# Performance work log

Measured on AMD Instinct MI355X. Metric: run time of the kernel, lower is better.

The kernel has to match this reference:

```python
import jax, jax.numpy as jnp
import numpy as np

V, E, H, K = 100000, 256, 512, 7
T, B = 256, 128


def _lstm(Wih, Whh, bih, bhh, xs):
    # xs: [T, B, E] -> hs: [T, B, H]. PyTorch gate order: i, f, g, o.
    Bsz = xs.shape[1]
    Hd = Whh.shape[1]
    b = bih + bhh

    def step(carry, x):
        h, c = carry
        gates = x @ Wih.T + h @ Whh.T + b  # [B, 4H]
        i, f, g, o = jnp.split(gates, 4, axis=-1)
        c = jax.nn.sigmoid(f) * c + jax.nn.sigmoid(i) * jnp.tanh(g)
        h = jax.nn.sigmoid(o) * jnp.tanh(c)
        return (h, c), h

    init = (jnp.zeros((Bsz, Hd), xs.dtype), jnp.zeros((Bsz, Hd), xs.dtype))
    _, hs = jax.lax.scan(step, init, xs)
    return hs


def setup_inputs() -> dict:
    key = jax.random.key(0)
    ks = jax.random.split(key, 16)
    s = 0.02
    n = lambda k, shape: (jax.random.normal(k, shape, dtype=jnp.float32) * s)
    inp = {
        "inputData": jax.random.randint(ks[0], (T, B), 0, V),
        "labels": jax.random.randint(ks[1], (B, T), 0, K),
        "embed_table": jax.random.normal(ks[2], (V, E), dtype=jnp.float32),
        "Wih_f": n(ks[3], (4 * H, E)), "Whh_f": n(ks[4], (4 * H, H)),
        "bih_f": n(ks[5], (4 * H,)), "bhh_f": n(ks[6], (4 * H,)),
        "Wih_b": n(ks[7], (4 * H, E)), "Whh_b": n(ks[8], (4 * H, H)),
        "bih_b": n(ks[9], (4 * H,)), "bhh_b": n(ks[10], (4 * H,)),
        "lin_W": n(ks[11], (K, 2 * H)), "lin_b": n(ks[12], (K,)),
        "trans": n(ks[13], (K, K)),
        "start_trans": n(ks[14], (K,)),
        "end_trans": n(ks[15], (K,)),
    }
    return inp


def reference(inputData, labels, embed_table, Wih_f, Whh_f, bih_f, bhh_f,
              Wih_b, Whh_b, bih_b, bhh_b, lin_W, lin_b, trans, start_trans, end_trans):
    # Embedding + BiLSTM (seq-major, torch default batch_first=False)
    xs = embed_table[inputData]                        # [T, B, E]
    hs_f = _lstm(Wih_f, Whh_f, bih_f, bhh_f, xs)       # [T, B, H]
    hs_b = _lstm(Wih_b, Whh_b, bih_b, bhh_b, xs[::-1])[::-1]
    hs = jnp.concatenate([hs_f, hs_b], axis=-1)        # [T, B, 2H]
    emissions = hs @ lin_W.T + lin_b                   # [T, B, K]

    em = emissions.transpose(1, 0, 2)                  # [B, T, K] batch-first for CRF

    # --- CRF gold-path score (mask = all ones, include start/end transitions) ---
    emit_scores = jnp.take_along_axis(em, labels[..., None], axis=2)[..., 0]  # [B, T]
    score = (start_trans[labels[:, 0]]
             + emit_scores.sum(axis=1)
             + trans[labels[:, :-1], labels[:, 1:]].sum(axis=1)
             + end_trans[labels[:, -1]])               # [B]

    # --- CRF log-partition via forward algorithm (lax.scan over time) ---
    alpha0 = start_trans[None, :] + em[:, 0]           # [B, K]

    def fwd_step(alpha, e_t):  # e_t: [B, K]
        new = jax.nn.logsumexp(alpha[:, :, None] + trans[None, :, :] + e_t[:, None, :], axis=1)
        return new, None

    alphaT, _ = jax.lax.scan(fwd_step, alpha0, em[:, 1:].transpose(1, 0, 2))
    logZ = jax.nn.logsumexp(alphaT + end_trans[None, :], axis=1)  # [B]

    log_likelihood = (score - logZ).sum()
    return -log_likelihood
```

## Files before the change

### kernel.cpp

```cpp
#include <hip/hip_runtime.h>
#include <hip/hip_bf16.h>

#define TT 256
#define BB 128
#define EE 256
#define HH 512
#define KK 7
#define WLD 776

typedef short bf16x8 __attribute__((ext_vector_type(8)));
typedef float f32x4 __attribute__((ext_vector_type(4)));
typedef unsigned short u16x8 __attribute__((ext_vector_type(8)));

__device__ __forceinline__ unsigned short f2bf(float x) {
  unsigned u = __builtin_bit_cast(unsigned, x);
  u += 0x7FFFu + ((u >> 16) & 1u);
  return (unsigned short)(u >> 16);
}
__device__ __forceinline__ float bf2f(unsigned short b) {
  return __builtin_bit_cast(float, (unsigned)b << 16);
}

__device__ __forceinline__ bf16x8 gload_sc0(const unsigned short* p) {
  bf16x8 v;
  asm volatile("global_load_dwordx4 %0, %1, off sc0"
               : "=v"(v) : "v"(p) : "memory");
  return v;
}

__global__ __launch_bounds__(256) void embed_kernel(
    const int* __restrict__ ids, const float* __restrict__ emb,
    unsigned short* __restrict__ xsb) {
  const int t = blockIdx.x, tid = threadIdx.x;
  const int b = tid >> 1, half = tid & 1;
  const int id = ids[t * BB + b];
  const float4* src = (const float4*)(emb + (size_t)id * EE + half * 128);
  unsigned short* dst = xsb + ((size_t)t * BB + b) * EE + half * 128;
#pragma unroll
  for (int i = 0; i < 32; ++i) {
    const float4 v = src[i];
    ushort4 o;
    o.x = f2bf(v.x); o.y = f2bf(v.y); o.z = f2bf(v.z); o.w = f2bf(v.w);
    *(ushort4*)(dst + i * 4) = o;
  }
}

__global__ __launch_bounds__(128) void bilstm_kernel(
    const unsigned short* __restrict__ xsb,
    const float* __restrict__ Wih_f, const float* __restrict__ Whh_f,
    const float* __restrict__ bih_f, const float* __restrict__ bhh_f,
    const float* __restrict__ Wih_b, const float* __restrict__ Whh_b,
    const float* __restrict__ bih_b, const float* __restrict__ bhh_b,
    unsigned short* __restrict__ hbuf, unsigned short* __restrict__ hs,
    int* __restrict__ bar) {
  __shared__ unsigned short Wl[64][WLD];
  __shared__ float gt[2][2][4][64][4];
  __shared__ int sinfo[2];

  const int tid = threadIdx.x;
  if (tid == 0) {
    const unsigned xcd = __builtin_amdgcn_s_getreg(14356) & 7;
    sinfo[0] = (int)xcd;
    sinfo[1] = atomicAdd(&bar[256 + xcd * 32], 1);
  }
  __syncthreads();
  const int g = sinfo[0];
  const int slot = sinfo[1] & 31;
  const int dir = g >> 2;
  const int r0 = (g & 3) * 32;
  const int j0 = slot * 16;
  int* cnt = bar + g * 32;

  const float* Wih = dir ? Wih_b : Wih_f;
  const float* Whh = dir ? Whh_b : Whh_f;
  const float* bih = dir ? bih_b : bih_f;
  const float* bhh = dir ? bhh_b : bhh_f;

  for (int idx = tid; idx < 64 * 192; idx += 128) {
    const int r = idx / 192;
    const int k4 = (idx - r * 192) * 4;
    const int grow = (r >> 4) * HH + j0 + (r & 15);
    float4 v;
    if (k4 < EE) v = *(const float4*)(Wih + (size_t)grow * EE + k4);
    else v = *(const float4*)(Whh + (size_t)grow * HH + (k4 - EE));
    ushort4 o;
    o.x = f2bf(v.x); o.y = f2bf(v.y); o.z = f2bf(v.z); o.w = f2bf(v.w);
    *(ushort4*)&Wl[r][k4] = o;
  }
  const int lane = tid & 63, ln = lane & 15, kk = lane >> 4;
  const int kh = tid >> 6;

  const float bi_ = bih[0 * HH + j0 + ln] + bhh[0 * HH + j0 + ln];
  const float bf_ = bih[1 * HH + j0 + ln] + bhh[1 * HH + j0 + ln];
  const float bg_ = bih[2 * HH + j0 + ln] + bhh[2 * HH + j0 + ln];
  const float bo_ = bih[3 * HH + j0 + ln] + bhh[3 * HH + j0 + ln];

  const unsigned short* wlp0 = &Wl[0 * 16 + ln][kk * 8];
  const unsigned short* wlp1 = &Wl[1 * 16 + ln][kk * 8];
  const unsigned short* wlp2 = &Wl[2 * 16 + ln][kk * 8];
  const unsigned short* wlp3 = &Wl[3 * 16 + ln][kk * 8];

  float c[4] = {0.f, 0.f, 0.f, 0.f};
  __syncthreads();

  int target = 32;
  for (int s = 0; s < TT; ++s) {
    const int t = dir ? (TT - 1 - s) : s;
    const int p = s & 1;
    f32x4 a00 = {0,0,0,0}, a01 = a00, a02 = a00, a03 = a00;
    f32x4 a10 = a00, a11 = a00, a12 = a00, a13 = a00;

    bf16x8 hv0[12], hv1[12];
    const unsigned short* hbase =
        hbuf + ((size_t)(p * 8 + g) * 32) * HH + kk * 8;
    const unsigned short* hp0 = hbase + (size_t)ln * HH;
    const unsigned short* hp1 = hbase + (size_t)(16 + ln) * HH;
    if (s > 0) {
      if (kh == 0) {
#pragma unroll
        for (int i = 0; i < 4; ++i) {
          hv0[i] = gload_sc0(hp0 + i * 32);
          hv1[i] = gload_sc0(hp1 + i * 32);
        }
      } else {
#pragma unroll
        for (int i = 0; i < 12; ++i) {
          hv0[i] = gload_sc0(hp0 + (4 + i) * 32);
          hv1[i] = gload_sc0(hp1 + (4 + i) * 32);
        }
      }
    }
    if (kh == 0) {
      const unsigned short* xr0 = xsb + ((size_t)t * BB + r0 + ln) * EE + kk * 8;
      const unsigned short* xr1 = xr0 + 16 * EE;
#pragma unroll
      for (int kt = 0; kt < 8; ++kt) {
        const bf16x8 av0 = *(const bf16x8*)(xr0 + kt * 32);
        const bf16x8 av1 = *(const bf16x8*)(xr1 + kt * 32);
        const bf16x8 b0 = *(const bf16x8*)(wlp0 + kt * 32);
        const bf16x8 b1 = *(const bf16x8*)(wlp1 + kt * 32);
        const bf16x8 b2 = *(const bf16x8*)(wlp2 + kt * 32);
        const bf16x8 b3 = *(const bf16x8*)(wlp3 + kt * 32);
        a00 = __builtin_amdgcn_mfma_f32_16x16x32_bf16(av0, b0, a00, 0, 0, 0);
        a01 = __builtin_amdgcn_mfma_f32_16x16x32_bf16(av0, b1, a01, 0, 0, 0);
        a02 = __builtin_amdgcn_mfma_f32_16x16x32_bf16(av0, b2, a02, 0, 0, 0);
        a03 = __builtin_amdgcn_mfma_f32_16x16x32_bf16(av0, b3, a03, 0, 0, 0);
        a10 = __builtin_amdgcn_mfma_f32_16x16x32_bf16(av1, b0, a10, 0, 0, 0);
        a11 = __builtin_amdgcn_mfma_f32_16x16x32_bf16(av1, b1, a11, 0, 0, 0);
        a12 = __builtin_amdgcn_mfma_f32_16x16x32_bf16(av1, b2, a12, 0, 0, 0);
        a13 = __builtin_amdgcn_mfma_f32_16x16x32_bf16(av1, b3, a13, 0, 0, 0);
      }
    }
    if (s > 0) {
      asm volatile("s_waitcnt vmcnt(0)" ::: "memory");
      __builtin_amdgcn_sched_barrier(0);
      if (kh == 0) {
#pragma unroll
        for (int i = 0; i < 4; ++i) {
          const int kt = i;
          const bf16x8 b0 = *(const bf16x8*)(wlp0 + EE + kt * 32);
          const bf16x8 b1 = *(const bf16x8*)(wlp1 + EE + kt * 32);
          const bf16x8 b2 = *(const bf16x8*)(wlp2 + EE + kt * 32);
          const bf16x8 b3 = *(const bf16x8*)(wlp3 + EE + kt * 32);
          a00 = __builtin_amdgcn_mfma_f32_16x16x32_bf16(hv0[i], b0, a00, 0, 0, 0);
          a01 = __builtin_amdgcn_mfma_f32_16x16x32_bf16(hv0[i], b1, a01, 0, 0, 0);
          a02 = __builtin_amdgcn_mfma_f32_16x16x32_bf16(hv0[i], b2, a02, 0, 0, 0);
          a03 = __builtin_amdgcn_mfma_f32_16x16x32_bf16(hv0[i], b3, a03, 0, 0, 0);
          a10 = __builtin_amdgcn_mfma_f32_16x16x32_bf16(hv1[i], b0, a10, 0, 0, 0);
          a11 = __builtin_amdgcn_mfma_f32_16x16x32_bf16(hv1[i], b1, a11, 0, 0, 0);
          a12 = __builtin_amdgcn_mfma_f32_16x16x32_bf16(hv1[i], b2, a12, 0, 0, 0);
          a13 = __builtin_amdgcn_mfma_f32_16x16x32_bf16(hv1[i], b3, a13, 0, 0, 0);
        }
      } else {
#pragma unroll
        for (int i = 0; i < 12; ++i) {
          const int kt = 4 + i;
          const bf16x8 b0 = *(const bf16x8*)(wlp0 + EE + kt * 32);
          const bf16x8 b1 = *(const bf16x8*)(wlp1 + EE + kt * 32);
          const bf16x8 b2 = *(const bf16x8*)(wlp2 + EE + kt * 32);
          const bf16x8 b3 = *(const bf16x8*)(wlp3 + EE + kt * 32);
          a00 = __builtin_amdgcn_mfma_f32_16x16x32_bf16(hv0[i], b0, a00, 0, 0, 0);
          a01 = __builtin_amdgcn_mfma_f32_16x16x32_bf16(hv0[i], b1, a01, 0, 0, 0);
          a02 = __builtin_amdgcn_mfma_f32_16x16x32_bf16(hv0[i], b2, a02, 0, 0, 0);
          a03 = __builtin_amdgcn_mfma_f32_16x16x32_bf16(hv0[i], b3, a03, 0, 0, 0);
          a10 = __builtin_amdgcn_mfma_f32_16x16x32_bf16(hv1[i], b0, a10, 0, 0, 0);
          a11 = __builtin_amdgcn_mfma_f32_16x16x32_bf16(hv1[i], b1, a11, 0, 0, 0);
          a12 = __builtin_amdgcn_mfma_f32_16x16x32_bf16(hv1[i], b2, a12, 0, 0, 0);
          a13 = __builtin_amdgcn_mfma_f32_16x16x32_bf16(hv1[i], b3, a13, 0, 0, 0);
        }
      }
    }
    *(f32x4*)&gt[kh][0][0][lane][0] = a00;
    *(f32x4*)&gt[kh][0][1][lane][0] = a01;
    *(f32x4*)&gt[kh][0][2][lane][0] = a02;
    *(f32x4*)&gt[kh][0][3][lane][0] = a03;
    *(f32x4*)&gt[kh][1][0][lane][0] = a10;
    *(f32x4*)&gt[kh][1][1][lane][0] = a11;
    *(f32x4*)&gt[kh][1][2][lane][0] = a12;
    *(f32x4*)&gt[kh][1][3][lane][0] = a13;
    __syncthreads();
    {
      const int mu = kh;
      unsigned short* hw =
          hbuf + ((size_t)((p ^ 1) * 8 + g) * 32 + mu * 16 + kk * 4) * HH + j0 + ln;
      unsigned short* hsw =
          hs + ((size_t)t * BB + r0 + mu * 16 + kk * 4) * 1024 + dir * HH + j0 + ln;
#pragma unroll
      for (int r = 0; r < 4; ++r) {
        const float gi = gt[0][mu][0][lane][r] + gt[1][mu][0][lane][r] + bi_;
        const float gf = gt[0][mu][1][lane][r] + gt[1][mu][1][lane][r] + bf_;
        const float gg = gt[0][mu][2][lane][r] + gt[1][mu][2][lane][r] + bg_;
        const float go = gt[0][mu][3][lane][r] + gt[1][mu][3][lane][r] + bo_;
        const float si = 1.f / (1.f + __expf(-gi));
        const float sf = 1.f / (1.f + __expf(-gf));
        const float so = 1.f / (1.f + __expf(-go));
        const float gcl = fminf(fmaxf(gg, -30.f), 30.f);
        const float eg = __expf(-2.f * gcl);
        const float tg = (1.f - eg) / (1.f + eg);
        const float cn = fmaf(sf, c[r], si * tg);
        c[r] = cn;
        const float ccl = fminf(fmaxf(cn, -30.f), 30.f);
        const float ec = __expf(-2.f * ccl);
        const float tc = (1.f - ec) / (1.f + ec);
        const float hn = so * tc;
        const unsigned short hb = f2bf(hn);
        hw[(size_t)r * HH] = hb;
        hsw[(size_t)r * 1024] = hb;
      }
    }
    __syncthreads();
    if (tid == 0) {
      __hip_atomic_fetch_add(cnt, 1, __ATOMIC_RELAXED, __HIP_MEMORY_SCOPE_AGENT);
      while (__hip_atomic_load(cnt, __ATOMIC_RELAXED, __HIP_MEMORY_SCOPE_AGENT) <
             target) {
        __builtin_amdgcn_s_sleep(1);
      }
    }
    __syncthreads();
    target += 32;
  }
}

__global__ __launch_bounds__(256) void emissions_kernel(
    const unsigned short* __restrict__ hs, const float* __restrict__ linW,
    const float* __restrict__ linb, float* __restrict__ em) {
  const int t = blockIdx.x, tid = threadIdx.x;
  const int wv = tid >> 6, l = tid & 63;
  for (int b = wv; b < BB; b += 4) {
    const unsigned short* hr = hs + ((size_t)t * BB + b) * 1024 + l * 16;
    const u16x8 v0 = *(const u16x8*)(hr);
    const u16x8 v1 = *(const u16x8*)(hr + 8);
    float x[16];
#pragma unroll
    for (int j = 0; j < 8; ++j) {
      x[j] = bf2f(v0[j]);
      x[8 + j] = bf2f(v1[j]);
    }
    float acc[KK];
#pragma unroll
    for (int k = 0; k < KK; ++k) {
      const float* wr = linW + (size_t)k * 1024 + l * 16;
      float ssum = 0.f;
#pragma unroll
      for (int j = 0; j < 16; ++j) ssum = fmaf(x[j], wr[j], ssum);
      acc[k] = ssum;
    }
#pragma unroll
    for (int k = 0; k < KK; ++k) {
#pragma unroll
      for (int off = 32; off > 0; off >>= 1) acc[k] += __shfl_xor(acc[k], off);
    }
    if (l == 0) {
      float* o = em + ((size_t)b * TT + t) * KK;
#pragma unroll
      for (int k = 0; k < KK; ++k) o[k] = acc[k] + linb[k];
    }
  }
}

__global__ __launch_bounds__(64) void crf_kernel(
    const float* __restrict__ em, const int* __restrict__ lab,
    const float* __restrict__ trans, const float* __restrict__ st_,
    const float* __restrict__ en_, float* __restrict__ partial) {
  const int b = blockIdx.x;
  const int lane = threadIdx.x;
  __shared__ float tr[49], st[7], en[7], al[2][7];
  if (lane < 49) tr[lane] = trans[lane];
  if (lane < 7) {
    st[lane] = st_[lane];
    en[lane] = en_[lane];
  }
  const float* e = em + (size_t)b * TT * KK;
  const int* lb = lab + (size_t)b * TT;
  if (lane < 7) al[0][lane] = st_[lane] + e[lane];
  __syncthreads();
  float gold = 0.f;
  int lp = lb[0];
  if (lane == 0) gold = st[lp] + e[lp];
  int p = 0;
  for (int t = 1; t < TT; ++t) {
    const float* et = e + t * KK;
    if (lane < 7) {
      float v[7], m = -1e30f;
#pragma unroll
      for (int k = 0; k < 7; ++k) {
        v[k] = al[p][k] + tr[k * 7 + lane];
        m = fmaxf(m, v[k]);
      }
      float ssum = 0.f;
#pragma unroll
      for (int k = 0; k < 7; ++k) ssum += __expf(v[k] - m);
      al[p ^ 1][lane] = m + __logf(ssum) + et[lane];
    }
    if (lane == 0) {
      const int lt = lb[t];
      gold += tr[lp * 7 + lt] + et[lt];
      lp = lt;
    }
    __syncthreads();
    p ^= 1;
  }
  if (lane == 0) {
    float m = -1e30f, v[7];
#pragma unroll
    for (int k = 0; k < 7; ++k) {
      v[k] = al[p][k] + en[k];
      m = fmaxf(m, v[k]);
    }
    float ssum = 0.f;
#pragma unroll
    for (int k = 0; k < 7; ++k) ssum += __expf(v[k] - m);
    partial[b] = (m + __logf(ssum)) - gold;
  }
}

__global__ __launch_bounds__(128) void reduce_kernel(const float* __restrict__ partial,
                                                     float* __restrict__ out) {
  __shared__ float r[128];
  const int tid = threadIdx.x;
  r[tid] = partial[tid];
  __syncthreads();
  for (int off = 64; off > 0; off >>= 1) {
    if (tid < off) r[tid] += r[tid + off];
    __syncthreads();
  }
  if (tid == 0) out[0] = r[0];
}

extern "C" void kernel_launch(void* const* d_in, const int* in_sizes, int n_in,
                              void* d_out, int out_size, void* d_ws, size_t ws_size,
                              hipStream_t stream) {
  const int* ids = (const int*)d_in[0];
  const int* lab = (const int*)d_in[1];
  const float* emb = (const float*)d_in[2];
  const float* Wih_f = (const float*)d_in[3];
  const float* Whh_f = (const float*)d_in[4];
  const float* bih_f = (const float*)d_in[5];
  const float* bhh_f = (const float*)d_in[6];
  const float* Wih_b = (const float*)d_in[7];
  const float* Whh_b = (const float*)d_in[8];
  const float* bih_b = (const float*)d_in[9];
  const float* bhh_b = (const float*)d_in[10];
  const float* linW = (const float*)d_in[11];
  const float* linb = (const float*)d_in[12];
  const float* trans = (const float*)d_in[13];
  const float* st = (const float*)d_in[14];
  const float* en = (const float*)d_in[15];
  float* out = (float*)d_out;

  char* ws = (char*)d_ws;
  int* bar = (int*)ws;
  unsigned short* xsb = (unsigned short*)(ws + 2048);
  unsigned short* hbuf = xsb + (size_t)TT * BB * EE;
  unsigned short* hs = hbuf + (size_t)2 * 8 * 32 * HH;
  float* em = (float*)(hs + (size_t)TT * BB * 1024);
  float* partial = em + (size_t)BB * TT * KK;

  hipMemsetAsync(bar, 0, 2048, stream);

  embed_kernel<<<dim3(TT), dim3(256), 0, stream>>>(ids, emb, xsb);

  void* args[] = {(void*)&xsb,   (void*)&Wih_f, (void*)&Whh_f, (void*)&bih_f,
                  (void*)&bhh_f, (void*)&Wih_b, (void*)&Whh_b, (void*)&bih_b,
                  (void*)&bhh_b, (void*)&hbuf,  (void*)&hs,    (void*)&bar};
  hipLaunchCooperativeKernel((void*)bilstm_kernel, dim3(256), dim3(128),
                             args, 0, stream);

  emissions_kernel<<<dim3(TT), dim3(256), 0, stream>>>(hs, linW, linb, em);
  crf_kernel<<<dim3(BB), dim3(64), 0, stream>>>(em, lab, trans, st, en, partial);
  reduce_kernel<<<dim3(1), dim3(128), 0, stream>>>(partial, out);
}
```

Before: 1.392 ms.

## Replace LSTM grid barrier with per-slot flags, prefetch x, warp-parallel CRF

The per-step counter barrier in the BiLSTM kernel is replaced by per-block progress flags: each block stores its step number and the next step polls all 32 flags of its group with a wave-wide check. The step flag is published before the hs store, so hs writes leave the critical path. The next timestep's input slice is prefetched into registers to overlap with the current step's MFMAs, and the gate reduction reads whole f32x4 rows from shared memory. The CRF kernel is rewritten to run the forward recursion with wave shuffles and bpermute instead of shared memory plus __syncthreads, and the gold score is computed in parallel across lanes. These changes add register pressure, and correctness depends on relaxed atomics plus sc0 loads giving the needed ordering.

```diff
diff --git a/kernel.cpp b/kernel.cpp
--- a/kernel.cpp
+++ b/kernel.cpp
@@ -23,8 +23,12 @@
 
 __device__ __forceinline__ bf16x8 gload_sc0(const unsigned short* p) {
   bf16x8 v;
-  asm volatile("global_load_dwordx4 %0, %1, off sc0"
-               : "=v"(v) : "v"(p) : "memory");
+  asm volatile("global_load_dwordx4 %0, %1, off sc0" : "=v"(v) : "v"(p) : "memory");
+  return v;
+}
+__device__ __forceinline__ bf16x8 gload16(const unsigned short* p) {
+  bf16x8 v;
+  asm volatile("global_load_dwordx4 %0, %1, off" : "=v"(v) : "v"(p) : "memory");
   return v;
 }
 
@@ -45,7 +49,7 @@
   }
 }
 
-__global__ __launch_bounds__(128) void bilstm_kernel(
+__global__ __launch_bounds__(128, 1) void bilstm_kernel(
     const unsigned short* __restrict__ xsb,
     const float* __restrict__ Wih_f, const float* __restrict__ Whh_f,
     const float* __restrict__ bih_f, const float* __restrict__ bhh_f,
@@ -54,14 +58,14 @@
     unsigned short* __restrict__ hbuf, unsigned short* __restrict__ hs,
     int* __restrict__ bar) {
   __shared__ unsigned short Wl[64][WLD];
-  __shared__ float gt[2][2][4][64][4];
+  __shared__ f32x4 gt[2][2][4][64];
   __shared__ int sinfo[2];
 
   const int tid = threadIdx.x;
   if (tid == 0) {
     const unsigned xcd = __builtin_amdgcn_s_getreg(14356) & 7;
     sinfo[0] = (int)xcd;
-    sinfo[1] = atomicAdd(&bar[256 + xcd * 32], 1);
+    sinfo[1] = atomicAdd(&bar[512 + xcd], 1);
   }
   __syncthreads();
   const int g = sinfo[0];
@@ -69,7 +73,7 @@
   const int dir = g >> 2;
   const int r0 = (g & 3) * 32;
   const int j0 = slot * 16;
-  int* cnt = bar + g * 32;
+  int* arr = bar + g * 64;
 
   const float* Wih = dir ? Wih_b : Wih_f;
   const float* Whh = dir ? Whh_b : Whh_f;
@@ -101,144 +105,142 @@
   const unsigned short* wlp3 = &Wl[3 * 16 + ln][kk * 8];
 
   float c[4] = {0.f, 0.f, 0.f, 0.f};
+
+  bf16x8 xc0[8], xc1[8];
+  if (kh == 0) {
+    const int t0 = dir ? TT - 1 : 0;
+    const unsigned short* xr0 = xsb + ((size_t)t0 * BB + r0 + ln) * EE + kk * 8;
+    const unsigned short* xr1 = xr0 + (size_t)16 * EE;
+#pragma unroll
+    for (int i = 0; i < 8; ++i) {
+      xc0[i] = *(const bf16x8*)(xr0 + i * 32);
+      xc1[i] = *(const bf16x8*)(xr1 + i * 32);
+    }
+  }
   __syncthreads();
 
-  int target = 32;
+#define MFMA8(AV0, AV1, OFF)                                               \
+  {                                                                        \
+    const bf16x8 b0 = *(const bf16x8*)(wlp0 + (OFF));                      \
+    const bf16x8 b1 = *(const bf16x8*)(wlp1 + (OFF));                      \
+    const bf16x8 b2 = *(const bf16x8*)(wlp2 + (OFF));                      \
+    const bf16x8 b3 = *(const bf16x8*)(wlp3 + (OFF));                      \
+    a00 = __builtin_amdgcn_mfma_f32_16x16x32_bf16(AV0, b0, a00, 0, 0, 0);  \
+    a01 = __builtin_amdgcn_mfma_f32_16x16x32_bf16(AV0, b1, a01, 0, 0, 0);  \
+    a02 = __builtin_amdgcn_mfma_f32_16x16x32_bf16(AV0, b2, a02, 0, 0, 0);  \
+    a03 = __builtin_amdgcn_mfma_f32_16x16x32_bf16(AV0, b3, a03, 0, 0, 0);  \
+    a10 = __builtin_amdgcn_mfma_f32_16x16x32_bf16(AV1, b0, a10, 0, 0, 0);  \
+    a11 = __builtin_amdgcn_mfma_f32_16x16x32_bf16(AV1, b1, a11, 0, 0, 0);  \
+    a12 = __builtin_amdgcn_mfma_f32_16x16x32_bf16(AV1, b2, a12, 0, 0, 0);  \
+    a13 = __builtin_amdgcn_mfma_f32_16x16x32_bf16(AV1, b3, a13, 0, 0, 0);  \
+  }
+
   for (int s = 0; s < TT; ++s) {
     const int t = dir ? (TT - 1 - s) : s;
     const int p = s & 1;
-    f32x4 a00 = {0,0,0,0}, a01 = a00, a02 = a00, a03 = a00;
+    if (s > 0) {
+      int fv;
+      do {
+        fv = __hip_atomic_load(&arr[lane & 31], __ATOMIC_RELAXED,
+                               __HIP_MEMORY_SCOPE_AGENT);
+      } while (!__all(fv >= s));
+    }
+    f32x4 a00 = {0.f, 0.f, 0.f, 0.f}, a01 = a00, a02 = a00, a03 = a00;
     f32x4 a10 = a00, a11 = a00, a12 = a00, a13 = a00;
-
-    bf16x8 hv0[12], hv1[12];
-    const unsigned short* hbase =
-        hbuf + ((size_t)(p * 8 + g) * 32) * HH + kk * 8;
+    bf16x8 hv0[12], hv1[12], xn0[8], xn1[8];
+    const unsigned short* hbase = hbuf + ((size_t)(p * 8 + g) * 32) * HH + kk * 8;
     const unsigned short* hp0 = hbase + (size_t)ln * HH;
     const unsigned short* hp1 = hbase + (size_t)(16 + ln) * HH;
-    if (s > 0) {
-      if (kh == 0) {
+
+    if (kh == 0) {
+      if (s > 0) {
 #pragma unroll
         for (int i = 0; i < 4; ++i) {
           hv0[i] = gload_sc0(hp0 + i * 32);
           hv1[i] = gload_sc0(hp1 + i * 32);
         }
-      } else {
+      }
+      if (s < TT - 1) {
+        const int t2 = dir ? t - 1 : t + 1;
+        const unsigned short* xr0 = xsb + ((size_t)t2 * BB + r0 + ln) * EE + kk * 8;
+        const unsigned short* xr1 = xr0 + (size_t)16 * EE;
+#pragma unroll
+        for (int i = 0; i < 8; ++i) {
+          xn0[i] = gload16(xr0 + i * 32);
+          xn1[i] = gload16(xr1 + i * 32);
+        }
+      }
+      if (s > 0) {
+        if (s < TT - 1) asm volatile("s_waitcnt vmcnt(16)" ::: "memory");
+        else            asm volatile("s_waitcnt vmcnt(0)" ::: "memory");
+        __builtin_amdgcn_sched_barrier(0);
+      }
+#pragma unroll
+      for (int kt = 0; kt < 8; ++kt) MFMA8(xc0[kt], xc1[kt], kt * 32);
+      if (s > 0) {
+#pragma unroll
+        for (int i = 0; i < 4; ++i) MFMA8(hv0[i], hv1[i], EE + i * 32);
+      }
+    } else {
+      if (s > 0) {
 #pragma unroll
         for (int i = 0; i < 12; ++i) {
           hv0[i] = gload_sc0(hp0 + (4 + i) * 32);
           hv1[i] = gload_sc0(hp1 + (4 + i) * 32);
         }
-      }
-    }
-    if (kh == 0) {
-      const unsigned short* xr0 = xsb + ((size_t)t * BB + r0 + ln) * EE + kk * 8;
-      const unsigned short* xr1 = xr0 + 16 * EE;
-#pragma unroll
-      for (int kt = 0; kt < 8; ++kt) {
-        const bf16x8 av0 = *(const bf16x8*)(xr0 + kt * 32);
-        const bf16x8 av1 = *(const bf16x8*)(xr1 + kt * 32);
-        const bf16x8 b0 = *(const bf16x8*)(wlp0 + kt * 32);
-        const bf16x8 b1 = *(const bf16x8*)(wlp1 + kt * 32);
-        const bf16x8 b2 = *(const bf16x8*)(wlp2 + kt * 32);
-        const bf16x8 b3 = *(const bf16x8*)(wlp3 + kt * 32);
-        a00 = __builtin_amdgcn_mfma_f32_16x16x32_bf16(av0, b0, a00, 0, 0, 0);
-        a01 = __builtin_amdgcn_mfma_f32_16x16x32_bf16(av0, b1, a01, 0, 0, 0);
-        a02 = __builtin_amdgcn_mfma_f32_16x16x32_bf16(av0, b2, a02, 0, 0, 0);
-        a03 = __builtin_amdgcn_mfma_f32_16x16x32_bf16(av0, b3, a03, 0, 0, 0);
-        a10 = __builtin_amdgcn_mfma_f32_16x16x32_bf16(av1, b0, a10, 0, 0, 0);
-        a11 = __builtin_amdgcn_mfma_f32_16x16x32_bf16(av1, b1, a11, 0, 0, 0);
-        a12 = __builtin_amdgcn_mfma_f32_16x16x32_bf16(av1, b2, a12, 0, 0, 0);
-        a13 = __builtin_amdgcn_mfma_f32_16x16x32_bf16(av1, b3, a13, 0, 0, 0);
-      }
-    }
-    if (s > 0) {
-      asm volatile("s_waitcnt vmcnt(0)" ::: "memory");
-      __builtin_amdgcn_sched_barrier(0);
-      if (kh == 0) {
-#pragma unroll
-        for (int i = 0; i < 4; ++i) {
-          const int kt = i;
-          const bf16x8 b0 = *(const bf16x8*)(wlp0 + EE + kt * 32);
-          const bf16x8 b1 = *(const bf16x8*)(wlp1 + EE + kt * 32);
-          const bf16x8 b2 = *(const bf16x8*)(wlp2 + EE + kt * 32);
-          const bf16x8 b3 = *(const bf16x8*)(wlp3 + EE + kt * 32);
-          a00 = __builtin_amdgcn_mfma_f32_16x16x32_bf16(hv0[i], b0, a00, 0, 0, 0);
-          a01 = __builtin_amdgcn_mfma_f32_16x16x32_bf16(hv0[i], b1, a01, 0, 0, 0);
-          a02 = __builtin_amdgcn_mfma_f32_16x16x32_bf16(hv0[i], b2, a02, 0, 0, 0);
-          a03 = __builtin_amdgcn_mfma_f32_16x16x32_bf16(hv0[i], b3, a03, 0, 0, 0);
-          a10 = __builtin_amdgcn_mfma_f32_16x16x32_bf16(hv1[i], b0, a10, 0, 0, 0);
-          a11 = __builtin_amdgcn_mfma_f32_16x16x32_bf16(hv1[i], b1, a11, 0, 0, 0);
-          a12 = __builtin_amdgcn_mfma_f32_16x16x32_bf16(hv1[i], b2, a12, 0, 0, 0);
-          a13 = __builtin_amdgcn_mfma_f32_16x16x32_bf16(hv1[i], b3, a13, 0, 0, 0);
-        }
-      } else {
-#pragma unroll
-        for (int i = 0; i < 12; ++i) {
-          const int kt = 4 + i;
-          const bf16x8 b0 = *(const bf16x8*)(wlp0 + EE + kt * 32);
-          const bf16x8 b1 = *(const bf16x8*)(wlp1 + EE + kt * 32);
-          const bf16x8 b2 = *(const bf16x8*)(wlp2 + EE + kt * 32);
-          const bf16x8 b3 = *(const bf16x8*)(wlp3 + EE + kt * 32);
-          a00 = __builtin_amdgcn_mfma_f32_16x16x32_bf16(hv0[i], b0, a00, 0, 0, 0);
-          a01 = __builtin_amdgcn_mfma_f32_16x16x32_bf16(hv0[i], b1, a01, 0, 0, 0);
-          a02 = __builtin_amdgcn_mfma_f32_16x16x32_bf16(hv0[i], b2, a02, 0, 0, 0);
-          a03 = __builtin_amdgcn_mfma_f32_16x16x32_bf16(hv0[i], b3, a03, 0, 0, 0);
-          a10 = __builtin_amdgcn_mfma_f32_16x16x32_bf16(hv1[i], b0, a10, 0, 0, 0);
-          a11 = __builtin_amdgcn_mfma_f32_16x16x32_bf16(hv1[i], b1, a11, 0, 0, 0);
-          a12 = __builtin_amdgcn_mfma_f32_16x16x32_bf16(hv1[i], b2, a12, 0, 0, 0);
-          a13 = __builtin_amdgcn_mfma_f32_16x16x32_bf16(hv1[i], b3, a13, 0, 0, 0);
-        }
-      }
-    }
-    *(f32x4*)&gt[kh][0][0][lane][0] = a00;
-    *(f32x4*)&gt[kh][0][1][lane][0] = a01;
-    *(f32x4*)&gt[kh][0][2][lane][0] = a02;
-    *(f32x4*)&gt[kh][0][3][lane][0] = a03;
-    *(f32x4*)&gt[kh][1][0][lane][0] = a10;
-    *(f32x4*)&gt[kh][1][1][lane][0] = a11;
-    *(f32x4*)&gt[kh][1][2][lane][0] = a12;
-    *(f32x4*)&gt[kh][1][3][lane][0] = a13;
+        asm volatile("s_waitcnt vmcnt(0)" ::: "memory");
+        __builtin_amdgcn_sched_barrier(0);
+#pragma unroll
+        for (int i = 0; i < 12; ++i) MFMA8(hv0[i], hv1[i], EE + (4 + i) * 32);
+      }
+    }
+    gt[kh][0][0][lane] = a00; gt[kh][0][1][lane] = a01;
+    gt[kh][0][2][lane] = a02; gt[kh][0][3][lane] = a03;
+    gt[kh][1][0][lane] = a10; gt[kh][1][1][lane] = a11;
+    gt[kh][1][2][lane] = a12; gt[kh][1][3][lane] = a13;
     __syncthreads();
-    {
-      const int mu = kh;
-      unsigned short* hw =
-          hbuf + ((size_t)((p ^ 1) * 8 + g) * 32 + mu * 16 + kk * 4) * HH + j0 + ln;
-      unsigned short* hsw =
-          hs + ((size_t)t * BB + r0 + mu * 16 + kk * 4) * 1024 + dir * HH + j0 + ln;
-#pragma unroll
-      for (int r = 0; r < 4; ++r) {
-        const float gi = gt[0][mu][0][lane][r] + gt[1][mu][0][lane][r] + bi_;
-        const float gf = gt[0][mu][1][lane][r] + gt[1][mu][1][lane][r] + bf_;
-        const float gg = gt[0][mu][2][lane][r] + gt[1][mu][2][lane][r] + bg_;
-        const float go = gt[0][mu][3][lane][r] + gt[1][mu][3][lane][r] + bo_;
-        const float si = 1.f / (1.f + __expf(-gi));
-        const float sf = 1.f / (1.f + __expf(-gf));
-        const float so = 1.f / (1.f + __expf(-go));
-        const float gcl = fminf(fmaxf(gg, -30.f), 30.f);
-        const float eg = __expf(-2.f * gcl);
-        const float tg = (1.f - eg) / (1.f + eg);
-        const float cn = fmaf(sf, c[r], si * tg);
-        c[r] = cn;
-        const float ccl = fminf(fmaxf(cn, -30.f), 30.f);
-        const float ec = __expf(-2.f * ccl);
-        const float tc = (1.f - ec) / (1.f + ec);
-        const float hn = so * tc;
-        const unsigned short hb = f2bf(hn);
-        hw[(size_t)r * HH] = hb;
-        hsw[(size_t)r * 1024] = hb;
-      }
+    const f32x4 gi4 = gt[0][kh][0][lane] + gt[1][kh][0][lane];
+    const f32x4 gf4 = gt[0][kh][1][lane] + gt[1][kh][1][lane];
+    const f32x4 gg4 = gt[0][kh][2][lane] + gt[1][kh][2][lane];
+    const f32x4 go4 = gt[0][kh][3][lane] + gt[1][kh][3][lane];
+    unsigned short hbs[4];
+    unsigned short* hw =
+        hbuf + (((size_t)((p ^ 1) * 8 + g) * 32) + kh * 16 + kk * 4) * HH + j0 + ln;
+#pragma unroll
+    for (int r = 0; r < 4; ++r) {
+      const float gi = gi4[r] + bi_;
+      const float gf = gf4[r] + bf_;
+      const float gg = gg4[r] + bg_;
+      const float go = go4[r] + bo_;
+      const float si = 1.f / (1.f + __expf(-gi));
+      const float sf = 1.f / (1.f + __expf(-gf));
+      const float so = 1.f / (1.f + __expf(-go));
+      const float gcl = fminf(fmaxf(gg, -30.f), 30.f);
+      const float eg = __expf(-2.f * gcl);
+      const float tg = (1.f - eg) / (1.f + eg);
+      const float cn = fmaf(sf, c[r], si * tg);
+      c[r] = cn;
+      const float ccl = fminf(fmaxf(cn, -30.f), 30.f);
+      const float ec = __expf(-2.f * ccl);
+      const float tc = (1.f - ec) / (1.f + ec);
+      const float hn = so * tc;
+      hbs[r] = f2bf(hn);
+      hw[(size_t)r * HH] = hbs[r];
     }
     __syncthreads();
-    if (tid == 0) {
-      __hip_atomic_fetch_add(cnt, 1, __ATOMIC_RELAXED, __HIP_MEMORY_SCOPE_AGENT);
-      while (__hip_atomic_load(cnt, __ATOMIC_RELAXED, __HIP_MEMORY_SCOPE_AGENT) <
-             target) {
-        __builtin_amdgcn_s_sleep(1);
-      }
-    }
-    __syncthreads();
-    target += 32;
-  }
+    if (tid == 0)
+      __hip_atomic_store(&arr[slot], s + 1, __ATOMIC_RELAXED,
+                         __HIP_MEMORY_SCOPE_AGENT);
+    unsigned short* hsw =
+        hs + ((size_t)t * BB + r0 + kh * 16 + kk * 4) * 1024 + dir * HH + j0 + ln;
+#pragma unroll
+    for (int r = 0; r < 4; ++r) hsw[(size_t)r * 1024] = hbs[r];
+    if (kh == 0 && s < TT - 1) {
+#pragma unroll
+      for (int i = 0; i < 8; ++i) { xc0[i] = xn0[i]; xc1[i] = xn1[i]; }
+    }
+  }
+#undef MFMA8
 }
 
 __global__ __launch_bounds__(256) void emissions_kernel(
@@ -282,55 +284,47 @@
     const float* __restrict__ em, const int* __restrict__ lab,
     const float* __restrict__ trans, const float* __restrict__ st_,
     const float* __restrict__ en_, float* __restrict__ partial) {
-  const int b = blockIdx.x;
-  const int lane = threadIdx.x;
-  __shared__ float tr[49], st[7], en[7], al[2][7];
-  if (lane < 49) tr[lane] = trans[lane];
-  if (lane < 7) {
-    st[lane] = st_[lane];
-    en[lane] = en_[lane];
-  }
+  const int b = blockIdx.x, lane = threadIdx.x;
   const float* e = em + (size_t)b * TT * KK;
   const int* lb = lab + (size_t)b * TT;
-  if (lane < 7) al[0][lane] = st_[lane] + e[lane];
-  __syncthreads();
-  float gold = 0.f;
-  int lp = lb[0];
-  if (lane == 0) gold = st[lp] + e[lp];
-  int p = 0;
+  float gp = 0.f;
+  for (int t = lane; t < TT; t += 64) {
+    const int lt = lb[t];
+    gp += e[t * KK + lt];
+    if (t > 0) gp += trans[lb[t - 1] * KK + lt];
+  }
+#pragma unroll
+  for (int o = 32; o; o >>= 1) gp += __shfl_xor(gp, o);
+  const int dst = lane >> 3, src = lane & 7;
+  const bool vs = (src < 7), vd = (dst < 7);
+  const float trv = (vs && vd) ? trans[src * KK + dst] : 0.f;
+  float alb = vs ? (st_[src] + e[src]) : -1e30f;
   for (int t = 1; t < TT; ++t) {
-    const float* et = e + t * KK;
-    if (lane < 7) {
-      float v[7], m = -1e30f;
-#pragma unroll
-      for (int k = 0; k < 7; ++k) {
-        v[k] = al[p][k] + tr[k * 7 + lane];
-        m = fmaxf(m, v[k]);
-      }
-      float ssum = 0.f;
-#pragma unroll
-      for (int k = 0; k < 7; ++k) ssum += __expf(v[k] - m);
-      al[p ^ 1][lane] = m + __logf(ssum) + et[lane];
-    }
-    if (lane == 0) {
-      const int lt = lb[t];
-      gold += tr[lp * 7 + lt] + et[lt];
-      lp = lt;
-    }
-    __syncthreads();
-    p ^= 1;
-  }
+    const float ev = vd ? e[t * KK + dst] : 0.f;
+    float v = vs ? (alb + trv) : -1e30f;
+    float mx = v;
+#pragma unroll
+    for (int o = 1; o < 8; o <<= 1) mx = fmaxf(mx, __shfl_xor(mx, o));
+    float sm = __expf(v - mx);
+#pragma unroll
+    for (int o = 1; o < 8; o <<= 1) sm += __shfl_xor(sm, o);
+    const float aln = mx + __logf(sm) + ev;
+    alb = __builtin_bit_cast(
+        float, __builtin_amdgcn_ds_bpermute((lane & 7) * 32,
+                                            __builtin_bit_cast(int, aln)));
+    if (!vs) alb = -1e30f;
+  }
+  float v = (lane < 7) ? (alb + en_[lane]) : -1e30f;
+  float mx = v;
+#pragma unroll
+  for (int o = 1; o < 8; o <<= 1) mx = fmaxf(mx, __shfl_xor(mx, o));
+  float sm = __expf(v - mx);
+#pragma unroll
+  for (int o = 1; o < 8; o <<= 1) sm += __shfl_xor(sm, o);
   if (lane == 0) {
-    float m = -1e30f, v[7];
-#pragma unroll
-    for (int k = 0; k < 7; ++k) {
-      v[k] = al[p][k] + en[k];
-      m = fmaxf(m, v[k]);
-    }
-    float ssum = 0.f;
-#pragma unroll
-    for (int k = 0; k < 7; ++k) ssum += __expf(v[k] - m);
-    partial[b] = (m + __logf(ssum)) - gold;
+    const float logZ = mx + __logf(sm);
+    const float gold = gp + st_[lb[0]] + en_[lb[TT - 1]];
+    partial[b] = logZ - gold;
   }
 }
 
@@ -370,13 +364,13 @@
 
   char* ws = (char*)d_ws;
   int* bar = (int*)ws;
-  unsigned short* xsb = (unsigned short*)(ws + 2048);
+  unsigned short* xsb = (unsigned short*)(ws + 4096);
   unsigned short* hbuf = xsb + (size_t)TT * BB * EE;
   unsigned short* hs = hbuf + (size_t)2 * 8 * 32 * HH;
   float* em = (float*)(hs + (size_t)TT * BB * 1024);
   float* partial = em + (size_t)BB * TT * KK;
 
-  hipMemsetAsync(bar, 0, 2048, stream);
+  hipMemsetAsync(bar, 0, 4096, stream);
 
   embed_kernel<<<dim3(TT), dim3(256), 0, stream>>>(ids, emb, xsb);
 
```

After: 1.444 ms. 1.04x slower.
